# Optimization experiments

Measured on AMD Instinct MI355X. Metric: run time of the kernel, lower is better.

Reference implementation:

```python
import jax, jax.numpy as jnp
import numpy as np

THETA = 10000.0
NUM_HEADS = 16


def _rope(x, positions):
    # x: [B, H, S, Dk] (fp32), positions: [B, S] int
    d_k = x.shape[-1]
    k = jnp.arange(0, d_k, 2, dtype=jnp.float32)
    freqs = THETA ** (-k / d_k)                      # [Dk/2]
    angles = positions[..., None].astype(jnp.float32) * freqs  # [B, S, Dk/2]
    cos = jnp.cos(angles)[:, None, :, :]             # [B, 1, S, Dk/2]
    sin = jnp.sin(angles)[:, None, :, :]
    xr = x.reshape(*x.shape[:-1], d_k // 2, 2)
    x_even, x_odd = xr[..., 0], xr[..., 1]
    rot_even = x_even * cos - x_odd * sin
    rot_odd = x_even * sin + x_odd * cos
    out = jnp.stack([rot_even, rot_odd], axis=-1)
    return out.reshape(x.shape)


def setup_inputs() -> dict:
    key = jax.random.key(0)
    ks = jax.random.split(key, 6)
    B, S, D = 2, 2048, 1024
    std = (2.0 / (D + D)) ** 0.5
    x = jax.random.normal(ks[0], (B, S, D), dtype=jnp.float32)
    Wq = jax.random.normal(ks[1], (D, D), dtype=jnp.float32) * std
    Wk = jax.random.normal(ks[2], (D, D), dtype=jnp.float32) * std
    Wv = jax.random.normal(ks[3], (D, D), dtype=jnp.float32) * std
    Wo = jax.random.normal(ks[4], (D, D), dtype=jnp.float32) * std
    token_positions = jnp.broadcast_to(jnp.arange(S, dtype=jnp.int32), (B, S))
    return {"x": x, "Wq": Wq, "Wk": Wk, "Wv": Wv, "Wo": Wo,
            "token_positions": token_positions}


def reference(x, Wq, Wk, Wv, Wo, token_positions):
    B, S, D = x.shape
    H = NUM_HEADS
    Dk = D // H
    # QKV projections (no bias): y = x @ W.T
    def proj(W):
        return (x @ W.T).reshape(B, S, H, Dk).transpose(0, 2, 1, 3)  # [B,H,S,Dk]
    Q, K, V = proj(Wq), proj(Wk), proj(Wv)
    Q = _rope(Q, token_positions)
    K = _rope(K, token_positions)
    scale = 1.0 / jnp.sqrt(jnp.float32(Dk))
    scores = jnp.einsum('bhqd,bhkd->bhqk', Q, K) * scale  # [B,H,S,S]
    causal = jnp.tril(jnp.ones((S, S), dtype=bool))
    scores = jnp.where(causal, scores, -jnp.inf)
    attn = jax.nn.softmax(scores.astype(jnp.float32), axis=-1)
    out = jnp.einsum('bhqk,bhkd->bhqd', attn, V)          # [B,H,S,Dk]
    out = out.transpose(0, 2, 1, 3).reshape(B, S, D)
    return out @ Wo.T
```

## Files before the change

kernel.cpp:

```cpp
#include <hip/hip_runtime.h>
#include <math.h>

#define D_MODEL 1024
#define NHEADS 16
#define DK 64
#define SEQ 2048
#define BATCH 2
#define MROWS (BATCH * SEQ)

typedef __attribute__((ext_vector_type(8))) short bfrag8;
typedef __attribute__((ext_vector_type(4))) float f32x4;
typedef unsigned short u16;
typedef __attribute__((ext_vector_type(8))) u16 u16x8;
typedef __attribute__((ext_vector_type(4))) u16 u16x4;

#define GLOBAL_AS(p) ((const __attribute__((address_space(1))) void*)(p))
#define LDS_AS(p)    ((__attribute__((address_space(3))) void*)(p))

#define RAW_BARRIER()  __asm__ volatile("s_barrier" ::: "memory")
#define WAIT_VM4()     __asm__ volatile("s_waitcnt vmcnt(4)" ::: "memory")
#define WAIT_VM0()     __asm__ volatile("s_waitcnt vmcnt(0)" ::: "memory")

__device__ inline u16 f2bf(float f) {
  union { float f; unsigned u; } c; c.f = f;
  unsigned r = c.u + 0x7FFF + ((c.u >> 16) & 1);
  return (u16)(r >> 16);
}

__device__ inline unsigned pack_bf2(float lo, float hi) {
  return __builtin_amdgcn_perm(__float_as_uint(hi), __float_as_uint(lo), 0x07060302);
}

struct CvtPtrs { const float* src[5]; };

__global__ __launch_bounds__(256)
void convert_and_tab(CvtPtrs p, u16* __restrict__ dst,
                     const int* __restrict__ pos, float2* __restrict__ tab) {
  const int bi = blockIdx.x;
  if (bi < 8192) {
    size_t base = ((size_t)bi * 256 + threadIdx.x) * 4;
    const size_t XSZ = (size_t)MROWS * D_MODEL;
    const float* s; size_t off;
    if (base < XSZ) { s = p.src[0]; off = base; }
    else {
      size_t j = base - XSZ;
      s = p.src[1 + (int)(j >> 20)];
      off = j & ((1u << 20) - 1);
    }
    float4 v = *(const float4*)(s + off);
    u16 o[4] = { f2bf(v.x), f2bf(v.y), f2bf(v.z), f2bf(v.w) };
    *(u16x4*)(dst + base) = *(u16x4*)o;
  } else {
    int idx = (bi - 8192) * 256 + threadIdx.x;
    int i = idx & 31, bs = idx >> 5;
    float pp = (float)pos[bs];
    float freq = expf(-(float)i * 0.2878231366242558f);
    float sn, cs;
    sincosf(pp * freq, &sn, &cs);
    tab[idx] = make_float2(cs, sn);
  }
}

__device__ inline void gemm_core(const u16* __restrict__ A, const u16* __restrict__ B,
                                 int m0, int n0, u16* As, u16* Bs,
                                 f32x4 acc[4][4]) {
  const int tid = threadIdx.x;
  const int w = tid >> 6, lane = tid & 63;
  const int l15 = lane & 15, quad = lane >> 4;
  const int wm = w >> 1, wn = w & 1;
  const int srow = tid >> 2;
  const int scol = (tid & 3) * 8;

  #pragma unroll
  for (int mi = 0; mi < 4; ++mi)
    #pragma unroll
    for (int ni = 0; ni < 4; ++ni) acc[mi][ni] = (f32x4)0.f;

  for (int k0 = 0; k0 < D_MODEL; k0 += 32) {
    __syncthreads();
    #pragma unroll
    for (int i = 0; i < 2; ++i) {
      const u16* ga = A + (size_t)((i * 64 + srow) + m0) * D_MODEL + k0 + scol;
      const u16* gb = B + (size_t)((i * 64 + srow) + n0) * D_MODEL + k0 + scol;
      __builtin_amdgcn_global_load_lds(GLOBAL_AS(ga), LDS_AS(&As[(i * 64 + w * 16) * 32]), 16, 0, 0);
      __builtin_amdgcn_global_load_lds(GLOBAL_AS(gb), LDS_AS(&Bs[(i * 64 + w * 16) * 32]), 16, 0, 0);
    }
    __syncthreads();

    bfrag8 af[4], bfr[4];
    #pragma unroll
    for (int i = 0; i < 4; ++i) {
      af[i]  = *(const bfrag8*)&As[(wm * 64 + i * 16 + l15) * 32 + quad * 8];
      bfr[i] = *(const bfrag8*)&Bs[(wn * 64 + i * 16 + l15) * 32 + quad * 8];
    }
    #pragma unroll
    for (int mi = 0; mi < 4; ++mi)
      #pragma unroll
      for (int ni = 0; ni < 4; ++ni)
        acc[mi][ni] = __builtin_amdgcn_mfma_f32_16x16x32_bf16(af[mi], bfr[ni], acc[mi][ni], 0, 0, 0);
  }
}

struct QKVArgs { const u16* A[3]; const u16* B[3]; u16* dst[3]; const float2* tab; };

__global__ __launch_bounds__(256)
void gemm_qkv_fused(QKVArgs p) {
  __shared__ u16 As[128 * 32];
  __shared__ u16 Bs[128 * 32];
  const int z = blockIdx.z;
  const int bi = blockIdx.x;
  int m0, n0;
  if (z < 2) { m0 = (bi & 7) * 128; n0 = (bi >> 3) * 128; }
  else       { m0 = (bi >> 3) * 128; n0 = (bi & 7) * 128; }
  f32x4 acc[4][4];
  gemm_core(p.A[z], p.B[z], m0, n0, As, Bs, acc);

  const int tid = threadIdx.x;
  const int w = tid >> 6, lane = tid & 63;
  const int l15 = lane & 15, quad = lane >> 4;
  const int wm = w >> 1, wn = w & 1;
  u16* dst = p.dst[z];

  if (z < 2) {
    const int head = (m0 + wm * 64) >> 6;
    const float scale = (z == 0) ? 0.125f * 1.4426950408889634f : 1.0f;
    #pragma unroll
    for (int ni = 0; ni < 4; ++ni) {
      int sg = n0 + wn * 64 + ni * 16 + l15;
      int b = sg >> 11;
      int s = sg & (SEQ - 1);
      size_t ho = ((size_t)(b * NHEADS + head)) * SEQ * DK;
      #pragma unroll
      for (int mi = 0; mi < 4; ++mi) {
        float4 t = *(const float4*)&p.tab[(size_t)sg * 32 + mi * 8 + quad * 2];
        float e0 = acc[mi][ni][0], o0 = acc[mi][ni][1];
        float e1 = acc[mi][ni][2], o1 = acc[mi][ni][3];
        u16x4 ov = { f2bf((e0 * t.x - o0 * t.y) * scale),
                     f2bf((e0 * t.y + o0 * t.x) * scale),
                     f2bf((e1 * t.z - o1 * t.w) * scale),
                     f2bf((e1 * t.w + o1 * t.z) * scale) };
        *(u16x4*)&dst[ho + (size_t)s * DK + mi * 16 + quad * 4] = ov;
      }
    }
  } else {
    const int b = m0 >> 11;
    const int head = (n0 >> 6) + wn;
    const size_t ho = ((size_t)(b * NHEADS + head)) * SEQ * DK;
    const int row_base = m0 + wm * 64;
    #pragma unroll
    for (int mi = 0; mi < 4; ++mi)
      #pragma unroll
      for (int ni = 0; ni < 4; ++ni) {
        int d = ni * 16 + l15;
        int sb = (row_base + mi * 16 + quad * 4) & (SEQ - 1);
        u16 o[4];
        #pragma unroll
        for (int r = 0; r < 4; ++r) o[r] = f2bf(acc[mi][ni][r]);
        *(u16x4*)&dst[ho + (size_t)d * SEQ + sb] = *(u16x4*)o;
      }
  }
}

__global__ __launch_bounds__(256)
void gemm_out_bf16(const u16* __restrict__ A, const u16* __restrict__ B,
                   float* __restrict__ C) {
  __shared__ u16 As[128 * 32];
  __shared__ u16 Bs[64 * 32];
  const int m0 = blockIdx.y * 128, n0 = blockIdx.x * 64;
  const int tid = threadIdx.x;
  const int w = tid >> 6, lane = tid & 63;
  const int l15 = lane & 15, quad = lane >> 4;
  const int wm = w >> 1, wn = w & 1;
  const int lrow = lane >> 2;
  const int lcol = (lane & 3) * 8;

  f32x4 acc[4][2];
  #pragma unroll
  for (int mi = 0; mi < 4; ++mi)
    #pragma unroll
    for (int ni = 0; ni < 2; ++ni) acc[mi][ni] = (f32x4)0.f;

  for (int k0 = 0; k0 < D_MODEL; k0 += 32) {
    __syncthreads();
    #pragma unroll
    for (int i = 0; i < 2; ++i) {
      int row = (i * 4 + w) * 16 + lrow;
      const u16* ga = A + (size_t)(m0 + row) * D_MODEL + k0 + lcol;
      __builtin_amdgcn_global_load_lds(GLOBAL_AS(ga), LDS_AS(&As[(i * 4 + w) * 16 * 32]), 16, 0, 0);
    }
    {
      int row = w * 16 + lrow;
      const u16* gb = B + (size_t)(n0 + row) * D_MODEL + k0 + lcol;
      __builtin_amdgcn_global_load_lds(GLOBAL_AS(gb), LDS_AS(&Bs[w * 16 * 32]), 16, 0, 0);
    }
    __syncthreads();

    bfrag8 af[4], bfr[2];
    #pragma unroll
    for (int i = 0; i < 4; ++i)
      af[i] = *(const bfrag8*)&As[(wm * 64 + i * 16 + l15) * 32 + quad * 8];
    #pragma unroll
    for (int i = 0; i < 2; ++i)
      bfr[i] = *(const bfrag8*)&Bs[(wn * 32 + i * 16 + l15) * 32 + quad * 8];
    #pragma unroll
    for (int mi = 0; mi < 4; ++mi)
      #pragma unroll
      for (int ni = 0; ni < 2; ++ni)
        acc[mi][ni] = __builtin_amdgcn_mfma_f32_16x16x32_bf16(af[mi], bfr[ni], acc[mi][ni], 0, 0, 0);
  }

  #pragma unroll
  for (int mi = 0; mi < 4; ++mi)
    #pragma unroll
    for (int ni = 0; ni < 2; ++ni)
      #pragma unroll
      for (int r = 0; r < 4; ++r) {
        int row = m0 + wm * 64 + mi * 16 + quad * 4 + r;
        int col = n0 + wn * 32 + ni * 16 + l15;
        C[(size_t)row * D_MODEL + col] = acc[mi][ni][r];
      }
}

__global__ __launch_bounds__(256, 4)
void attn_mfma(const u16* __restrict__ Qbf, const u16* __restrict__ Kbf,
               const u16* __restrict__ Vtb, u16* __restrict__ obb) {
  __shared__ u16 Ks[2][64 * 64];
  __shared__ u16 Vt[2][64 * 64];

  const int tid = threadIdx.x;
  const int w = tid >> 6, lane = tid & 63;
  const int l15 = lane & 15, quad = lane >> 4;

  const int bid = blockIdx.x;
  const int hb = bid & 31;
  const int g  = bid >> 5;
  const int tt = (g & 7) | ((g & 16) >> 1);
  const int qt = (g & 8) ? (31 - tt) : tt;
  const int b = hb >> 4, h = hb & 15;
  const size_t ho = (size_t)hb * SEQ * DK;
  const int qrow_base = qt * 64 + w * 16;

  bfrag8 qf[2];
  #pragma unroll
  for (int hh = 0; hh < 2; ++hh)
    qf[hh] = *(const bfrag8*)&Qbf[ho + (size_t)(qrow_base + l15) * DK + hh * 32 + quad * 8];

  f32x4 oacc[4];
  float l_ = 0.f;
  #pragma unroll
  for (int n0 = 0; n0 < 4; ++n0) oacc[n0] = (f32x4)0.f;

  const int srow = w * 8 + (lane >> 3);
  const int scc = ((lane & 7) ^ (srow & 7)) * 8;

  const int adr0 = (((quad & 1) << 5) + l15) << 2;
  const int adr1 = adr0 + 64;

  #define STAGE(T, BUF) do {                                                         \
    int j0_ = (T) * 64;                                                              \
    _Pragma("unroll")                                                                \
    for (int r_ = 0; r_ < 2; ++r_) {                                                 \
      int row_ = r_ * 32 + srow;                                                     \
      __builtin_amdgcn_global_load_lds(GLOBAL_AS(Kbf + ho + (size_t)(j0_ + row_) * DK + scc), \
                                       LDS_AS(&Ks[BUF][(r_ * 32 + w * 8) * 64]), 16, 0, 0);   \
      __builtin_amdgcn_global_load_lds(GLOBAL_AS(Vtb + ho + (size_t)row_ * SEQ + j0_ + scc),  \
                                       LDS_AS(&Vt[BUF][(r_ * 32 + w * 8) * 64]), 16, 0, 0);   \
    }                                                                                \
  } while (0)

  const int ntiles = qt + 1;
  STAGE(0, 0);

  for (int t = 0; t < ntiles; ++t) {
    const int j0 = t * 64;
    const int buf = t & 1;
    RAW_BARRIER();
    if (t + 1 < ntiles) {
      STAGE(t + 1, buf ^ 1);
      WAIT_VM4();
    } else {
      WAIT_VM0();
    }
    RAW_BARRIER();

    f32x4 sc[4];
    const int sw = l15 & 7;
    #pragma unroll
    for (int st = 0; st < 4; ++st) {
      int key = st * 16 + l15;
      bfrag8 kf0 = *(const bfrag8*)&Ks[buf][key * 64 + ((quad ^ sw) * 8)];
      bfrag8 kf1 = *(const bfrag8*)&Ks[buf][key * 64 + (((4 + quad) ^ sw) * 8)];
      sc[st] = __builtin_amdgcn_mfma_f32_16x16x32_bf16(kf0, qf[0], (f32x4)0.f, 0, 0, 0);
      sc[st] = __builtin_amdgcn_mfma_f32_16x16x32_bf16(kf1, qf[1], sc[st], 0, 0, 0);
    }

    if (j0 + 63 > qrow_base) {
      #pragma unroll
      for (int st = 0; st < 4; ++st)
        #pragma unroll
        for (int r = 0; r < 4; ++r) {
          int key = j0 + st * 16 + quad * 4 + r;
          if (key > qrow_base + l15) sc[st][r] = -60.f;
        }
    }

    unsigned pk[4][2];
    float rs = 0.f;
    #pragma unroll
    for (int st = 0; st < 4; ++st) {
      float p0 = __builtin_amdgcn_exp2f(fminf(sc[st][0], 60.f));
      float p1 = __builtin_amdgcn_exp2f(fminf(sc[st][1], 60.f));
      float p2 = __builtin_amdgcn_exp2f(fminf(sc[st][2], 60.f));
      float p3 = __builtin_amdgcn_exp2f(fminf(sc[st][3], 60.f));
      rs += (p0 + p1) + (p2 + p3);
      pk[st][0] = pack_bf2(p0, p1);
      pk[st][1] = pack_bf2(p2, p3);
    }
    l_ += rs;

    union PU { bfrag8 f; int i[4]; } u0, u1;
    #pragma unroll
    for (int j = 0; j < 4; ++j) {
      const int adr = (j & 2) ? adr1 : adr0;
      int lo0 = __builtin_amdgcn_ds_bpermute(adr, (int)pk[0][j & 1]);
      int hi0 = __builtin_amdgcn_ds_bpermute(adr, (int)pk[1][j & 1]);
      int lo1 = __builtin_amdgcn_ds_bpermute(adr, (int)pk[2][j & 1]);
      int hi1 = __builtin_amdgcn_ds_bpermute(adr, (int)pk[3][j & 1]);
      u0.i[j] = (quad & 2) ? hi0 : lo0;
      u1.i[j] = (quad & 2) ? hi1 : lo1;
    }
    bfrag8 pf[2] = { u0.f, u1.f };

    #pragma unroll
    for (int n0 = 0; n0 < 4; ++n0) {
      #pragma unroll
      for (int kc = 0; kc < 2; ++kc) {
        bfrag8 vf = *(const bfrag8*)&Vt[buf][(n0 * 16 + l15) * 64 + (((kc * 4 + quad) ^ sw) * 8)];
        oacc[n0] = __builtin_amdgcn_mfma_f32_16x16x32_bf16(vf, pf[kc], oacc[n0], 0, 0, 0);
      }
    }
  }
  #undef STAGE

  float l = l_;
  l += __shfl_xor(l, 16);
  l += __shfl_xor(l, 32);
  float inv = 1.f / l;
  int q = qrow_base + l15;
  #pragma unroll
  for (int n0 = 0; n0 < 4; ++n0) {
    u16x4 ov = { f2bf(oacc[n0][0] * inv), f2bf(oacc[n0][1] * inv),
                 f2bf(oacc[n0][2] * inv), f2bf(oacc[n0][3] * inv) };
    *(u16x4*)&obb[(size_t)(b * SEQ + q) * D_MODEL + h * DK + n0 * 16 + quad * 4] = ov;
  }
}

extern "C" void kernel_launch(void* const* d_in, const int* in_sizes, int n_in,
                              void* d_out, int out_size, void* d_ws, size_t ws_size,
                              hipStream_t stream) {
  const float* x  = (const float*)d_in[0];
  const float* Wq = (const float*)d_in[1];
  const float* Wk = (const float*)d_in[2];
  const float* Wv = (const float*)d_in[3];
  const float* Wo = (const float*)d_in[4];
  const int* pos  = (const int*)d_in[5];

  const size_t XSZ = (size_t)MROWS * D_MODEL;
  const size_t WSZ = (size_t)D_MODEL * D_MODEL;

  u16* bfb = (u16*)d_ws;
  u16* xb  = bfb;
  u16* wqb = xb  + XSZ;
  u16* wkb = wqb + WSZ;
  u16* wvb = wkb + WSZ;
  u16* wob = wvb + WSZ;
  u16* Qbf = wob + WSZ;
  u16* Kbf = Qbf + XSZ;
  u16* Vtb = Kbf + XSZ;
  u16* obb = Vtb + XSZ;
  float2* tab = (float2*)(obb + XSZ);

  CvtPtrs cp; cp.src[0] = x; cp.src[1] = Wq; cp.src[2] = Wk; cp.src[3] = Wv; cp.src[4] = Wo;
  convert_and_tab<<<8192 + 512, 256, 0, stream>>>(cp, xb, pos, tab);

  QKVArgs qp;
  qp.A[0] = wqb; qp.A[1] = wkb; qp.A[2] = xb;
  qp.B[0] = xb;  qp.B[1] = xb;  qp.B[2] = wvb;
  qp.dst[0] = Qbf; qp.dst[1] = Kbf; qp.dst[2] = Vtb;
  qp.tab = tab;
  gemm_qkv_fused<<<dim3(256, 1, 3), 256, 0, stream>>>(qp);

  attn_mfma<<<dim3(1024), 256, 0, stream>>>(Qbf, Kbf, Vtb, obb);

  gemm_out_bf16<<<dim3(D_MODEL / 64, MROWS / 128), 256, 0, stream>>>(obb, wob, (float*)d_out);
}
```

Baseline: 182.7 us.

## Double-buffer LDS tiles in QKV and output GEMMs to overlap loads with MFMA

Both projection GEMMs now use two LDS buffers per operand. The next K-slice is issued with global_load_lds before the current slice is consumed, and a partial vmcnt wait lets loads for tile t+1 stay in flight while MFMAs run on tile t. This targets the exposed global-load latency between the two barriers of each K step. The cost is doubled LDS use per block, which may lower occupancy, and it relies on raw barriers with hand-counted vmcnt values matching the number of loads issued per stage.

```diff
diff --git a/kernel.cpp b/kernel.cpp
--- a/kernel.cpp
+++ b/kernel.cpp
@@ -19,6 +19,7 @@
 
 #define RAW_BARRIER()  __asm__ volatile("s_barrier" ::: "memory")
 #define WAIT_VM4()     __asm__ volatile("s_waitcnt vmcnt(4)" ::: "memory")
+#define WAIT_VM3()     __asm__ volatile("s_waitcnt vmcnt(3)" ::: "memory")
 #define WAIT_VM0()     __asm__ volatile("s_waitcnt vmcnt(0)" ::: "memory")
 
 __device__ inline u16 f2bf(float f) {
@@ -76,22 +77,36 @@
     #pragma unroll
     for (int ni = 0; ni < 4; ++ni) acc[mi][ni] = (f32x4)0.f;
 
-  for (int k0 = 0; k0 < D_MODEL; k0 += 32) {
-    __syncthreads();
-    #pragma unroll
-    for (int i = 0; i < 2; ++i) {
-      const u16* ga = A + (size_t)((i * 64 + srow) + m0) * D_MODEL + k0 + scol;
-      const u16* gb = B + (size_t)((i * 64 + srow) + n0) * D_MODEL + k0 + scol;
-      __builtin_amdgcn_global_load_lds(GLOBAL_AS(ga), LDS_AS(&As[(i * 64 + w * 16) * 32]), 16, 0, 0);
-      __builtin_amdgcn_global_load_lds(GLOBAL_AS(gb), LDS_AS(&Bs[(i * 64 + w * 16) * 32]), 16, 0, 0);
-    }
-    __syncthreads();
+  #define GSTAGE(K0, BUF) do {                                                       \
+    _Pragma("unroll")                                                                \
+    for (int i_ = 0; i_ < 2; ++i_) {                                                 \
+      const u16* ga_ = A + (size_t)((i_ * 64 + srow) + m0) * D_MODEL + (K0) + scol;  \
+      const u16* gb_ = B + (size_t)((i_ * 64 + srow) + n0) * D_MODEL + (K0) + scol;  \
+      __builtin_amdgcn_global_load_lds(GLOBAL_AS(ga_),                               \
+          LDS_AS(&As[(BUF) * 4096 + (i_ * 64 + w * 16) * 32]), 16, 0, 0);            \
+      __builtin_amdgcn_global_load_lds(GLOBAL_AS(gb_),                               \
+          LDS_AS(&Bs[(BUF) * 4096 + (i_ * 64 + w * 16) * 32]), 16, 0, 0);            \
+    }                                                                                \
+  } while (0)
+
+  const int NT = D_MODEL / 32;
+  GSTAGE(0, 0);
+  for (int t = 0; t < NT; ++t) {
+    const int buf = t & 1;
+    RAW_BARRIER();
+    if (t + 1 < NT) {
+      GSTAGE((t + 1) * 32, buf ^ 1);
+      WAIT_VM4();
+    } else {
+      WAIT_VM0();
+    }
+    RAW_BARRIER();
 
     bfrag8 af[4], bfr[4];
     #pragma unroll
     for (int i = 0; i < 4; ++i) {
-      af[i]  = *(const bfrag8*)&As[(wm * 64 + i * 16 + l15) * 32 + quad * 8];
-      bfr[i] = *(const bfrag8*)&Bs[(wn * 64 + i * 16 + l15) * 32 + quad * 8];
+      af[i]  = *(const bfrag8*)&As[buf * 4096 + (wm * 64 + i * 16 + l15) * 32 + quad * 8];
+      bfr[i] = *(const bfrag8*)&Bs[buf * 4096 + (wn * 64 + i * 16 + l15) * 32 + quad * 8];
     }
     #pragma unroll
     for (int mi = 0; mi < 4; ++mi)
@@ -99,14 +114,15 @@
       for (int ni = 0; ni < 4; ++ni)
         acc[mi][ni] = __builtin_amdgcn_mfma_f32_16x16x32_bf16(af[mi], bfr[ni], acc[mi][ni], 0, 0, 0);
   }
+  #undef GSTAGE
 }
 
 struct QKVArgs { const u16* A[3]; const u16* B[3]; u16* dst[3]; const float2* tab; };
 
 __global__ __launch_bounds__(256)
 void gemm_qkv_fused(QKVArgs p) {
-  __shared__ u16 As[128 * 32];
-  __shared__ u16 Bs[128 * 32];
+  __shared__ u16 As[2 * 128 * 32];
+  __shared__ u16 Bs[2 * 128 * 32];
   const int z = blockIdx.z;
   const int bi = blockIdx.x;
   int m0, n0;
@@ -164,8 +180,8 @@
 __global__ __launch_bounds__(256)
 void gemm_out_bf16(const u16* __restrict__ A, const u16* __restrict__ B,
                    float* __restrict__ C) {
-  __shared__ u16 As[128 * 32];
-  __shared__ u16 Bs[64 * 32];
+  __shared__ u16 As[2 * 128 * 32];
+  __shared__ u16 Bs[2 * 64 * 32];
   const int m0 = blockIdx.y * 128, n0 = blockIdx.x * 64;
   const int tid = threadIdx.x;
   const int w = tid >> 6, lane = tid & 63;
@@ -180,34 +196,49 @@
     #pragma unroll
     for (int ni = 0; ni < 2; ++ni) acc[mi][ni] = (f32x4)0.f;
 
-  for (int k0 = 0; k0 < D_MODEL; k0 += 32) {
-    __syncthreads();
-    #pragma unroll
-    for (int i = 0; i < 2; ++i) {
-      int row = (i * 4 + w) * 16 + lrow;
-      const u16* ga = A + (size_t)(m0 + row) * D_MODEL + k0 + lcol;
-      __builtin_amdgcn_global_load_lds(GLOBAL_AS(ga), LDS_AS(&As[(i * 4 + w) * 16 * 32]), 16, 0, 0);
-    }
-    {
-      int row = w * 16 + lrow;
-      const u16* gb = B + (size_t)(n0 + row) * D_MODEL + k0 + lcol;
-      __builtin_amdgcn_global_load_lds(GLOBAL_AS(gb), LDS_AS(&Bs[w * 16 * 32]), 16, 0, 0);
-    }
-    __syncthreads();
+  #define OSTAGE(K0, BUF) do {                                                       \
+    _Pragma("unroll")                                                                \
+    for (int i_ = 0; i_ < 2; ++i_) {                                                 \
+      int row_ = (i_ * 4 + w) * 16 + lrow;                                           \
+      const u16* ga_ = A + (size_t)(m0 + row_) * D_MODEL + (K0) + lcol;              \
+      __builtin_amdgcn_global_load_lds(GLOBAL_AS(ga_),                               \
+          LDS_AS(&As[(BUF) * 4096 + (i_ * 4 + w) * 16 * 32]), 16, 0, 0);             \
+    }                                                                                \
+    {                                                                                \
+      int row_ = w * 16 + lrow;                                                      \
+      const u16* gb_ = B + (size_t)(n0 + row_) * D_MODEL + (K0) + lcol;              \
+      __builtin_amdgcn_global_load_lds(GLOBAL_AS(gb_),                               \
+          LDS_AS(&Bs[(BUF) * 2048 + w * 16 * 32]), 16, 0, 0);                        \
+    }                                                                                \
+  } while (0)
+
+  const int NT = D_MODEL / 32;
+  OSTAGE(0, 0);
+  for (int t = 0; t < NT; ++t) {
+    const int buf = t & 1;
+    RAW_BARRIER();
+    if (t + 1 < NT) {
+      OSTAGE((t + 1) * 32, buf ^ 1);
+      WAIT_VM3();
+    } else {
+      WAIT_VM0();
+    }
+    RAW_BARRIER();
 
     bfrag8 af[4], bfr[2];
     #pragma unroll
     for (int i = 0; i < 4; ++i)
-      af[i] = *(const bfrag8*)&As[(wm * 64 + i * 16 + l15) * 32 + quad * 8];
+      af[i] = *(const bfrag8*)&As[buf * 4096 + (wm * 64 + i * 16 + l15) * 32 + quad * 8];
     #pragma unroll
     for (int i = 0; i < 2; ++i)
-      bfr[i] = *(const bfrag8*)&Bs[(wn * 32 + i * 16 + l15) * 32 + quad * 8];
+      bfr[i] = *(const bfrag8*)&Bs[buf * 2048 + (wn * 32 + i * 16 + l15) * 32 + quad * 8];
     #pragma unroll
     for (int mi = 0; mi < 4; ++mi)
       #pragma unroll
       for (int ni = 0; ni < 2; ++ni)
         acc[mi][ni] = __builtin_amdgcn_mfma_f32_16x16x32_bf16(af[mi], bfr[ni], acc[mi][ni], 0, 0, 0);
   }
+  #undef OSTAGE
 
   #pragma unroll
   for (int mi = 0; mi < 4; ++mi)
```

After: 188.4 us. 3.1% more time.

## Fuse Q/K/V projections into one block sharing x tile with double-buffered loads

Applied to the files above, without the earlier changes.

The QKV kernel now computes all three projections in a single block, so each x tile is loaded into LDS once and reused against the Wq, Wk and Wv tiles. It also double-buffers the LDS stages, using raw barriers and vmcnt waits so the next tile's loads overlap the current tile's MFMAs. The V output is written transposed with scalar stores in a new layout. The grid shrinks from 768 to 256 blocks with 48 accumulators per thread and launch_bounds(256,1), which risks low occupancy and poor CU fill.

```diff
diff --git a/kernel.cpp b/kernel.cpp
--- a/kernel.cpp
+++ b/kernel.cpp
@@ -18,6 +18,7 @@
 #define LDS_AS(p)    ((__attribute__((address_space(3))) void*)(p))
 
 #define RAW_BARRIER()  __asm__ volatile("s_barrier" ::: "memory")
+#define WAIT_VM8()     __asm__ volatile("s_waitcnt vmcnt(8)" ::: "memory")
 #define WAIT_VM4()     __asm__ volatile("s_waitcnt vmcnt(4)" ::: "memory")
 #define WAIT_VM0()     __asm__ volatile("s_waitcnt vmcnt(0)" ::: "memory")
 
@@ -61,9 +62,20 @@
   }
 }
 
-__device__ inline void gemm_core(const u16* __restrict__ A, const u16* __restrict__ B,
-                                 int m0, int n0, u16* As, u16* Bs,
-                                 f32x4 acc[4][4]) {
+struct QKVFArgs {
+  const u16* Wq; const u16* Wk; const u16* Wv; const u16* x;
+  u16* dq; u16* dk; u16* dv; const float2* tab;
+};
+
+__global__ __launch_bounds__(256, 1)
+void gemm_qkv_fused(QKVFArgs p) {
+  __shared__ u16 As[3][2][128 * 32];
+  __shared__ u16 Bs[2][128 * 32];
+
+  const int bi = blockIdx.x;
+  const int m0 = (bi & 7) * 128;
+  const int n0 = (bi >> 3) * 128;
+
   const int tid = threadIdx.x;
   const int w = tid >> 6, lane = tid & 63;
   const int l15 = lane & 15, quad = lane >> 4;
@@ -71,92 +83,96 @@
   const int srow = tid >> 2;
   const int scol = (tid & 3) * 8;
 
-  #pragma unroll
-  for (int mi = 0; mi < 4; ++mi)
-    #pragma unroll
-    for (int ni = 0; ni < 4; ++ni) acc[mi][ni] = (f32x4)0.f;
-
-  for (int k0 = 0; k0 < D_MODEL; k0 += 32) {
-    __syncthreads();
-    #pragma unroll
-    for (int i = 0; i < 2; ++i) {
-      const u16* ga = A + (size_t)((i * 64 + srow) + m0) * D_MODEL + k0 + scol;
-      const u16* gb = B + (size_t)((i * 64 + srow) + n0) * D_MODEL + k0 + scol;
-      __builtin_amdgcn_global_load_lds(GLOBAL_AS(ga), LDS_AS(&As[(i * 64 + w * 16) * 32]), 16, 0, 0);
-      __builtin_amdgcn_global_load_lds(GLOBAL_AS(gb), LDS_AS(&Bs[(i * 64 + w * 16) * 32]), 16, 0, 0);
-    }
-    __syncthreads();
-
-    bfrag8 af[4], bfr[4];
-    #pragma unroll
-    for (int i = 0; i < 4; ++i) {
-      af[i]  = *(const bfrag8*)&As[(wm * 64 + i * 16 + l15) * 32 + quad * 8];
-      bfr[i] = *(const bfrag8*)&Bs[(wn * 64 + i * 16 + l15) * 32 + quad * 8];
-    }
+  f32x4 acc[3][4][4];
+  #pragma unroll
+  for (int z = 0; z < 3; ++z)
     #pragma unroll
     for (int mi = 0; mi < 4; ++mi)
       #pragma unroll
-      for (int ni = 0; ni < 4; ++ni)
-        acc[mi][ni] = __builtin_amdgcn_mfma_f32_16x16x32_bf16(af[mi], bfr[ni], acc[mi][ni], 0, 0, 0);
-  }
-}
-
-struct QKVArgs { const u16* A[3]; const u16* B[3]; u16* dst[3]; const float2* tab; };
-
-__global__ __launch_bounds__(256)
-void gemm_qkv_fused(QKVArgs p) {
-  __shared__ u16 As[128 * 32];
-  __shared__ u16 Bs[128 * 32];
-  const int z = blockIdx.z;
-  const int bi = blockIdx.x;
-  int m0, n0;
-  if (z < 2) { m0 = (bi & 7) * 128; n0 = (bi >> 3) * 128; }
-  else       { m0 = (bi >> 3) * 128; n0 = (bi & 7) * 128; }
-  f32x4 acc[4][4];
-  gemm_core(p.A[z], p.B[z], m0, n0, As, Bs, acc);
-
-  const int tid = threadIdx.x;
-  const int w = tid >> 6, lane = tid & 63;
-  const int l15 = lane & 15, quad = lane >> 4;
-  const int wm = w >> 1, wn = w & 1;
-  u16* dst = p.dst[z];
-
-  if (z < 2) {
-    const int head = (m0 + wm * 64) >> 6;
+      for (int ni = 0; ni < 4; ++ni) acc[z][mi][ni] = (f32x4)0.f;
+
+  #define FSTAGE(K0, BUF) do {                                                       \
+    _Pragma("unroll")                                                                \
+    for (int i_ = 0; i_ < 2; ++i_) {                                                 \
+      size_t ao_ = (size_t)((i_ * 64 + srow) + m0) * D_MODEL + (K0) + scol;          \
+      size_t bo_ = (size_t)((i_ * 64 + srow) + n0) * D_MODEL + (K0) + scol;          \
+      int ld_ = (i_ * 64 + w * 16) * 32;                                             \
+      __builtin_amdgcn_global_load_lds(GLOBAL_AS(p.Wq + ao_), LDS_AS(&As[0][BUF][ld_]), 16, 0, 0); \
+      __builtin_amdgcn_global_load_lds(GLOBAL_AS(p.Wk + ao_), LDS_AS(&As[1][BUF][ld_]), 16, 0, 0); \
+      __builtin_amdgcn_global_load_lds(GLOBAL_AS(p.Wv + ao_), LDS_AS(&As[2][BUF][ld_]), 16, 0, 0); \
+      __builtin_amdgcn_global_load_lds(GLOBAL_AS(p.x  + bo_), LDS_AS(&Bs[BUF][ld_]), 16, 0, 0);    \
+    }                                                                                \
+  } while (0)
+
+  const int NT = D_MODEL / 32;
+  FSTAGE(0, 0);
+  for (int t = 0; t < NT; ++t) {
+    const int buf = t & 1;
+    RAW_BARRIER();
+    if (t + 1 < NT) {
+      FSTAGE((t + 1) * 32, buf ^ 1);
+      WAIT_VM8();
+    } else {
+      WAIT_VM0();
+    }
+    RAW_BARRIER();
+
+    bfrag8 bfr[4];
+    #pragma unroll
+    for (int i = 0; i < 4; ++i)
+      bfr[i] = *(const bfrag8*)&Bs[buf][(wn * 64 + i * 16 + l15) * 32 + quad * 8];
+    #pragma unroll
+    for (int z = 0; z < 3; ++z) {
+      bfrag8 af[4];
+      #pragma unroll
+      for (int i = 0; i < 4; ++i)
+        af[i] = *(const bfrag8*)&As[z][buf][(wm * 64 + i * 16 + l15) * 32 + quad * 8];
+      #pragma unroll
+      for (int mi = 0; mi < 4; ++mi)
+        #pragma unroll
+        for (int ni = 0; ni < 4; ++ni)
+          acc[z][mi][ni] = __builtin_amdgcn_mfma_f32_16x16x32_bf16(af[mi], bfr[ni], acc[z][mi][ni], 0, 0, 0);
+    }
+  }
+  #undef FSTAGE
+
+  const int head = (m0 >> 6) + wm;
+  const int bB = n0 >> 11;
+  const size_t hoQ = ((size_t)(bB * NHEADS + head)) * SEQ * DK;
+
+  #pragma unroll
+  for (int z = 0; z < 2; ++z) {
+    u16* dst = z ? p.dk : p.dq;
     const float scale = (z == 0) ? 0.125f * 1.4426950408889634f : 1.0f;
     #pragma unroll
     for (int ni = 0; ni < 4; ++ni) {
       int sg = n0 + wn * 64 + ni * 16 + l15;
-      int b = sg >> 11;
       int s = sg & (SEQ - 1);
-      size_t ho = ((size_t)(b * NHEADS + head)) * SEQ * DK;
       #pragma unroll
       for (int mi = 0; mi < 4; ++mi) {
         float4 t = *(const float4*)&p.tab[(size_t)sg * 32 + mi * 8 + quad * 2];
-        float e0 = acc[mi][ni][0], o0 = acc[mi][ni][1];
-        float e1 = acc[mi][ni][2], o1 = acc[mi][ni][3];
+        float e0 = acc[z][mi][ni][0], o0 = acc[z][mi][ni][1];
+        float e1 = acc[z][mi][ni][2], o1 = acc[z][mi][ni][3];
         u16x4 ov = { f2bf((e0 * t.x - o0 * t.y) * scale),
                      f2bf((e0 * t.y + o0 * t.x) * scale),
                      f2bf((e1 * t.z - o1 * t.w) * scale),
                      f2bf((e1 * t.w + o1 * t.z) * scale) };
-        *(u16x4*)&dst[ho + (size_t)s * DK + mi * 16 + quad * 4] = ov;
+        *(u16x4*)&dst[hoQ + (size_t)s * DK + mi * 16 + quad * 4] = ov;
       }
     }
-  } else {
-    const int b = m0 >> 11;
-    const int head = (n0 >> 6) + wn;
-    const size_t ho = ((size_t)(b * NHEADS + head)) * SEQ * DK;
-    const int row_base = m0 + wm * 64;
+  }
+
+  {
+    const int sl_base = (n0 & (SEQ - 1)) + wn * 64;
     #pragma unroll
     for (int mi = 0; mi < 4; ++mi)
       #pragma unroll
-      for (int ni = 0; ni < 4; ++ni) {
-        int d = ni * 16 + l15;
-        int sb = (row_base + mi * 16 + quad * 4) & (SEQ - 1);
-        u16 o[4];
+      for (int r = 0; r < 4; ++r) {
+        int d = mi * 16 + quad * 4 + r;
+        u16* row = p.dv + hoQ + (size_t)d * SEQ;
         #pragma unroll
-        for (int r = 0; r < 4; ++r) o[r] = f2bf(acc[mi][ni][r]);
-        *(u16x4*)&dst[ho + (size_t)d * SEQ + sb] = *(u16x4*)o;
+        for (int ni = 0; ni < 4; ++ni)
+          row[sl_base + ni * 16 + l15] = f2bf(acc[2][mi][ni][r]);
       }
   }
 }
@@ -383,12 +399,11 @@
   CvtPtrs cp; cp.src[0] = x; cp.src[1] = Wq; cp.src[2] = Wk; cp.src[3] = Wv; cp.src[4] = Wo;
   convert_and_tab<<<8192 + 512, 256, 0, stream>>>(cp, xb, pos, tab);
 
-  QKVArgs qp;
-  qp.A[0] = wqb; qp.A[1] = wkb; qp.A[2] = xb;
-  qp.B[0] = xb;  qp.B[1] = xb;  qp.B[2] = wvb;
-  qp.dst[0] = Qbf; qp.dst[1] = Kbf; qp.dst[2] = Vtb;
+  QKVFArgs qp;
+  qp.Wq = wqb; qp.Wk = wkb; qp.Wv = wvb; qp.x = xb;
+  qp.dq = Qbf; qp.dk = Kbf; qp.dv = Vtb;
   qp.tab = tab;
-  gemm_qkv_fused<<<dim3(256, 1, 3), 256, 0, stream>>>(qp);
+  gemm_qkv_fused<<<dim3(256), 256, 0, stream>>>(qp);
 
   attn_mfma<<<dim3(1024), 256, 0, stream>>>(Qbf, Kbf, Vtb, obb);
 
```

Measured after the change: 204.1 us. +11.7%, slower.

## Double-buffer x tile in LDS and load weight fragments directly from global

Applied to the files above, without the earlier changes.

Rewrites the fused QKV GEMM. Only the x tile is staged in LDS, now double-buffered with async global-to-LDS loads. Each wave reads its weight fragments straight from global memory into registers one k-step ahead, and the old two-syncthreads-per-step loop becomes a raw-barrier ping-pong with vmcnt waits. This is meant to overlap loads with MFMA work and halve LDS traffic, with launch bounds hinting three blocks per CU. The cost is uncoalesced 16-byte global loads for weights, more register pressure, and correctness that depends on the hand-tuned vmcnt counts.

```diff
diff --git a/kernel.cpp b/kernel.cpp
--- a/kernel.cpp
+++ b/kernel.cpp
@@ -18,6 +18,7 @@
 #define LDS_AS(p)    ((__attribute__((address_space(3))) void*)(p))
 
 #define RAW_BARRIER()  __asm__ volatile("s_barrier" ::: "memory")
+#define WAIT_VM6()     __asm__ volatile("s_waitcnt vmcnt(6)" ::: "memory")
 #define WAIT_VM4()     __asm__ volatile("s_waitcnt vmcnt(4)" ::: "memory")
 #define WAIT_VM0()     __asm__ volatile("s_waitcnt vmcnt(0)" ::: "memory")
 
@@ -61,9 +62,18 @@
   }
 }
 
-__device__ inline void gemm_core(const u16* __restrict__ A, const u16* __restrict__ B,
-                                 int m0, int n0, u16* As, u16* Bs,
-                                 f32x4 acc[4][4]) {
+struct QKVArgs2 { const u16* W[3]; const u16* x; u16* dst[3]; const float2* tab; };
+
+__global__ __launch_bounds__(256, 3)
+void gemm_qkv(QKVArgs2 p) {
+  __shared__ u16 Xs[2][128 * 32];
+
+  const int z = blockIdx.z;
+  const int bi = blockIdx.x;
+  int m0, n0;
+  if (z < 2) { m0 = (bi & 7) * 128; n0 = (bi >> 3) * 128; }
+  else       { m0 = (bi >> 3) * 128; n0 = (bi & 7) * 128; }
+
   const int tid = threadIdx.x;
   const int w = tid >> 6, lane = tid & 63;
   const int l15 = lane & 15, quad = lane >> 4;
@@ -71,54 +81,79 @@
   const int srow = tid >> 2;
   const int scol = (tid & 3) * 8;
 
+  const int x0 = (z < 2) ? n0 : m0;
+  const int wrow = ((z < 2) ? (m0 + wm * 64) : (n0 + wn * 64)) + l15;
+  const int xg = (z < 2) ? wn : wm;
+  const u16* Wp = p.W[z];
+
+  f32x4 acc[4][4];
   #pragma unroll
   for (int mi = 0; mi < 4; ++mi)
     #pragma unroll
     for (int ni = 0; ni < 4; ++ni) acc[mi][ni] = (f32x4)0.f;
 
-  for (int k0 = 0; k0 < D_MODEL; k0 += 32) {
-    __syncthreads();
-    #pragma unroll
-    for (int i = 0; i < 2; ++i) {
-      const u16* ga = A + (size_t)((i * 64 + srow) + m0) * D_MODEL + k0 + scol;
-      const u16* gb = B + (size_t)((i * 64 + srow) + n0) * D_MODEL + k0 + scol;
-      __builtin_amdgcn_global_load_lds(GLOBAL_AS(ga), LDS_AS(&As[(i * 64 + w * 16) * 32]), 16, 0, 0);
-      __builtin_amdgcn_global_load_lds(GLOBAL_AS(gb), LDS_AS(&Bs[(i * 64 + w * 16) * 32]), 16, 0, 0);
-    }
-    __syncthreads();
-
-    bfrag8 af[4], bfr[4];
-    #pragma unroll
-    for (int i = 0; i < 4; ++i) {
-      af[i]  = *(const bfrag8*)&As[(wm * 64 + i * 16 + l15) * 32 + quad * 8];
-      bfr[i] = *(const bfrag8*)&Bs[(wn * 64 + i * 16 + l15) * 32 + quad * 8];
-    }
-    #pragma unroll
-    for (int mi = 0; mi < 4; ++mi)
-      #pragma unroll
-      for (int ni = 0; ni < 4; ++ni)
-        acc[mi][ni] = __builtin_amdgcn_mfma_f32_16x16x32_bf16(af[mi], bfr[ni], acc[mi][ni], 0, 0, 0);
-  }
-}
-
-struct QKVArgs { const u16* A[3]; const u16* B[3]; u16* dst[3]; const float2* tab; };
-
-__global__ __launch_bounds__(256)
-void gemm_qkv_fused(QKVArgs p) {
-  __shared__ u16 As[128 * 32];
-  __shared__ u16 Bs[128 * 32];
-  const int z = blockIdx.z;
-  const int bi = blockIdx.x;
-  int m0, n0;
-  if (z < 2) { m0 = (bi & 7) * 128; n0 = (bi >> 3) * 128; }
-  else       { m0 = (bi >> 3) * 128; n0 = (bi & 7) * 128; }
-  f32x4 acc[4][4];
-  gemm_core(p.A[z], p.B[z], m0, n0, As, Bs, acc);
-
-  const int tid = threadIdx.x;
-  const int w = tid >> 6, lane = tid & 63;
-  const int l15 = lane & 15, quad = lane >> 4;
-  const int wm = w >> 1, wn = w & 1;
+  #define XSTAGE(T, BUF) do {                                                        \
+    _Pragma("unroll")                                                                \
+    for (int i_ = 0; i_ < 2; ++i_) {                                                 \
+      const u16* gx_ = p.x + (size_t)(x0 + i_ * 64 + srow) * D_MODEL + (T) * 32 + scol; \
+      __builtin_amdgcn_global_load_lds(GLOBAL_AS(gx_),                               \
+          LDS_AS(&Xs[BUF][(i_ * 64 + w * 16) * 32]), 16, 0, 0);                      \
+    }                                                                                \
+  } while (0)
+
+  #define LOADWF(WF, T) do {                                                         \
+    _Pragma("unroll")                                                                \
+    for (int i_ = 0; i_ < 4; ++i_)                                                   \
+      WF[i_] = *(const bfrag8*)&Wp[(size_t)(wrow + i_ * 16) * D_MODEL + (T) * 32 + quad * 8]; \
+  } while (0)
+
+  #define COMPUTE(BUF, WF) do {                                                      \
+    bfrag8 xf_[4];                                                                   \
+    _Pragma("unroll")                                                                \
+    for (int i_ = 0; i_ < 4; ++i_)                                                   \
+      xf_[i_] = *(const bfrag8*)&Xs[BUF][(xg * 64 + i_ * 16 + l15) * 32 + quad * 8]; \
+    if (z < 2) {                                                                     \
+      _Pragma("unroll")                                                              \
+      for (int mi_ = 0; mi_ < 4; ++mi_)                                              \
+        _Pragma("unroll")                                                            \
+        for (int ni_ = 0; ni_ < 4; ++ni_)                                            \
+          acc[mi_][ni_] = __builtin_amdgcn_mfma_f32_16x16x32_bf16(WF[mi_], xf_[ni_], acc[mi_][ni_], 0, 0, 0); \
+    } else {                                                                         \
+      _Pragma("unroll")                                                              \
+      for (int mi_ = 0; mi_ < 4; ++mi_)                                              \
+        _Pragma("unroll")                                                            \
+        for (int ni_ = 0; ni_ < 4; ++ni_)                                            \
+          acc[mi_][ni_] = __builtin_amdgcn_mfma_f32_16x16x32_bf16(xf_[mi_], WF[ni_], acc[mi_][ni_], 0, 0, 0); \
+    }                                                                                \
+  } while (0)
+
+  const int NT = D_MODEL / 32;
+  bfrag8 wfA[4], wfB[4];
+  XSTAGE(0, 0);
+  LOADWF(wfA, 0);
+  #pragma unroll 1
+  for (int t = 0; t < NT; t += 2) {
+    RAW_BARRIER();
+    XSTAGE(t + 1, 1);
+    LOADWF(wfB, t + 1);
+    WAIT_VM6();
+    RAW_BARRIER();
+    COMPUTE(0, wfA);
+    RAW_BARRIER();
+    if (t + 2 < NT) {
+      XSTAGE(t + 2, 0);
+      LOADWF(wfA, t + 2);
+      WAIT_VM6();
+    } else {
+      WAIT_VM0();
+    }
+    RAW_BARRIER();
+    COMPUTE(1, wfB);
+  }
+  #undef XSTAGE
+  #undef LOADWF
+  #undef COMPUTE
+
   u16* dst = p.dst[z];
 
   if (z < 2) {
@@ -383,12 +418,11 @@
   CvtPtrs cp; cp.src[0] = x; cp.src[1] = Wq; cp.src[2] = Wk; cp.src[3] = Wv; cp.src[4] = Wo;
   convert_and_tab<<<8192 + 512, 256, 0, stream>>>(cp, xb, pos, tab);
 
-  QKVArgs qp;
-  qp.A[0] = wqb; qp.A[1] = wkb; qp.A[2] = xb;
-  qp.B[0] = xb;  qp.B[1] = xb;  qp.B[2] = wvb;
+  QKVArgs2 qp;
+  qp.W[0] = wqb; qp.W[1] = wkb; qp.W[2] = wvb; qp.x = xb;
   qp.dst[0] = Qbf; qp.dst[1] = Kbf; qp.dst[2] = Vtb;
   qp.tab = tab;
-  gemm_qkv_fused<<<dim3(256, 1, 3), 256, 0, stream>>>(qp);
+  gemm_qkv<<<dim3(256, 1, 3), 256, 0, stream>>>(qp);
 
   attn_mfma<<<dim3(1024), 256, 0, stream>>>(Qbf, Kbf, Vtb, obb);
 
```

Result: slower. 306.2 us (+67.6%).
